# Optimization experiments

Measured on AMD Instinct MI355X. Metric: run time of the kernel, lower is better.

The kernel has to match this reference:

```python
import jax, jax.numpy as jnp
import numpy as np

C = 0.1          # curvature
EPS = 1e-8
BN_EPS = 1e-5
MAX_NORM = 0.9

def batchnorm_train(x, gamma, beta):
    mu = jnp.mean(x, axis=0)
    var = jnp.var(x, axis=0)  # biased, matches torch BN normalization
    return gamma * (x - mu) * jax.lax.rsqrt(var + BN_EPS) + beta

def euclidean_to_poincare(x, c=C, max_norm=MAX_NORM):
    norm = jnp.linalg.norm(x, axis=-1, keepdims=True)
    zeros_mask = norm == 0
    safe_norm = jnp.where(zeros_mask, jnp.ones_like(norm), norm)
    sqrt_c = jnp.sqrt(jnp.asarray(c, x.dtype))
    scale = max_norm * jnp.tanh(sqrt_c * norm) / (sqrt_c * safe_norm)
    return jnp.where(zeros_mask, jnp.zeros_like(x), scale * x)

def poincare_to_euclidean(x, c=C):
    norms = jnp.linalg.norm(x, axis=-1, keepdims=True)
    norms = jnp.clip(norms, 1e-8, 1.0 - 1e-8)
    sqrt_c = jnp.sqrt(jnp.asarray(c, x.dtype))
    return x * jnp.arctanh(sqrt_c * norms) / (sqrt_c * norms)

def batch_poincare_exp_map(x, v, c=C):
    x_nsq = jnp.sum(x * x, axis=-1, keepdims=True)
    lambda_x = 2.0 / (1.0 - c * x_nsq + EPS)
    v_norm = jnp.linalg.norm(v, axis=-1, keepdims=True)
    v_norm = jnp.maximum(v_norm, EPS)
    sqrt_c = jnp.sqrt(jnp.asarray(c, x.dtype))
    scale = jnp.tanh(sqrt_c * lambda_x * v_norm / 2.0) / (sqrt_c * v_norm)
    sv = scale * v
    numerator = (1.0 - c * x_nsq) * sv
    x_sv = jnp.sum(x * sv, axis=-1, keepdims=True)
    sv_nsq = jnp.sum(sv * sv, axis=-1, keepdims=True)
    denom = 1.0 - 2.0 * c * x_sv + c * c * x_nsq * sv_nsq
    result = x + numerator / (denom + EPS)
    mask = jnp.all(jnp.isfinite(result), axis=-1, keepdims=True)
    return jnp.where(mask, result, jnp.zeros_like(result))

def batch_poincare_log_map(x, y, c=C):
    x_nsq = jnp.sum(x * x, axis=-1, keepdims=True)
    lambda_x = 2.0 / (1.0 - c * x_nsq + EPS)
    y_nsq = jnp.sum(y * y, axis=-1, keepdims=True)
    xy = jnp.sum(x * y, axis=-1, keepdims=True)
    numerator = (1.0 - 2.0 * c * xy + c * y_nsq) * x - (1.0 - c * x_nsq) * y
    denom = 1.0 - 2.0 * c * xy + c * c * x_nsq * y_nsq
    diff = numerator / (denom + EPS)
    diff_norm = jnp.linalg.norm(diff, axis=-1, keepdims=True)
    diff_norm = jnp.maximum(diff_norm, EPS)
    sqrt_c = jnp.sqrt(jnp.asarray(c, x.dtype))
    return 2.0 / (sqrt_c * lambda_x) * jnp.arctanh(sqrt_c * diff_norm) * diff / diff_norm

def setup_inputs() -> dict:
    key = jax.random.key(0)
    ks = jax.random.split(key, 8)
    B, D_IN, H, D_OUT = 8192, 1024, 2048, 1000
    x = jax.random.normal(ks[0], (B, D_IN), dtype=jnp.float32)
    # kaiming_normal fan_out: std = sqrt(2/fan_out) with fan_out = out_features
    W1 = jax.random.normal(ks[1], (H, D_IN), dtype=jnp.float32) * np.sqrt(2.0 / H)
    b1 = jnp.zeros((H,), jnp.float32)
    g1 = jnp.ones((H,), jnp.float32)
    be1 = jnp.zeros((H,), jnp.float32)
    W2 = jax.random.normal(ks[2], (H, H), dtype=jnp.float32) * np.sqrt(2.0 / H)
    b2 = jnp.zeros((H,), jnp.float32)
    g2 = jnp.ones((H,), jnp.float32)
    be2 = jnp.zeros((H,), jnp.float32)
    W3 = jax.random.normal(ks[3], (D_OUT, H), dtype=jnp.float32) * np.sqrt(2.0 / D_OUT)
    b3 = jnp.zeros((D_OUT,), jnp.float32)
    return {"x": x, "W1": W1, "b1": b1, "g1": g1, "be1": be1,
            "W2": W2, "b2": b2, "g2": g2, "be2": be2, "W3": W3, "b3": b3}

def reference(x, W1, b1, g1, be1, W2, b2, g2, be2, W3, b3):
    h1 = jax.nn.relu(batchnorm_train(x @ W1.T + b1, g1, be1))
    h1_hyp = euclidean_to_poincare(h1)
    origin = jnp.zeros_like(h1_hyp)
    h1_tan = batch_poincare_log_map(origin, h1_hyp)
    h2_tan = jax.nn.relu(batchnorm_train(h1_tan @ W2.T + b2, g2, be2))
    h2_hyp = batch_poincare_exp_map(origin, h2_tan)
    h2_euc = poincare_to_euclidean(h2_hyp)
    out = h2_euc @ W3.T + b3
    return jax.nn.log_softmax(out, axis=1)
```

## Files before the change

### kernel.cpp

```cpp
#include <hip/hip_runtime.h>

typedef __bf16 bf16x8 __attribute__((ext_vector_type(8)));
typedef float f32x16 __attribute__((ext_vector_type(16)));
typedef unsigned short us8 __attribute__((ext_vector_type(8)));

#define AS1 __attribute__((address_space(1)))
#define AS3 __attribute__((address_space(3)))

__device__ __forceinline__ unsigned short f2bf(float x) {
  unsigned int u = __float_as_uint(x);
  u += 0x7fffu + ((u >> 16) & 1u);
  return (unsigned short)(u >> 16);
}
__device__ __forceinline__ float bf2f(unsigned short u) {
  return __uint_as_float(((unsigned int)u) << 16);
}
__device__ __forceinline__ void async_copy16(const void* g, void* l) {
  __builtin_amdgcn_global_load_lds((AS1 void*)(g), (AS3 void*)(l), 16, 0, 0);
}

#define BARRIER() asm volatile("s_barrier" ::: "memory")
#define WAITV(n) asm volatile("s_waitcnt vmcnt(" #n ")" ::: "memory")

__global__ void __launch_bounds__(256) k_prep(const float* __restrict__ x,
                                              const float* __restrict__ W1,
                                              const float* __restrict__ W2,
                                              const float* __restrict__ W3,
                                              unsigned short* __restrict__ Xb,
                                              unsigned short* __restrict__ W1b,
                                              unsigned short* __restrict__ W2b,
                                              unsigned short* __restrict__ W3b,
                                              float* __restrict__ P) {
  const long n1 = 2097152, n2 = 524288, n3 = 1048576, n4 = 524288;
  long i = (long)blockIdx.x * 256 + threadIdx.x;
  const float* s = nullptr;
  unsigned short* d = nullptr;
  long j = i;
  if (i < n1)                { s = x;  d = Xb; }
  else if ((j -= n1) < n2)   { s = W1; d = W1b; }
  else if ((j -= n2) < n3)   { s = W2; d = W2b; }
  else if ((j -= n3) < n4) {
    ushort4 o;
    if ((j >> 9) < 1000) {
      float4 v = ((const float4*)W3)[j];
      o.x = f2bf(v.x); o.y = f2bf(v.y); o.z = f2bf(v.z); o.w = f2bf(v.w);
    } else { o.x = 0; o.y = 0; o.z = 0; o.w = 0; }
    ((ushort4*)W3b)[j] = o;
    return;
  } else {
    j -= n4;
    ((float4*)P)[j] = (float4){0.f, 0.f, 0.f, 0.f};
    return;
  }
  float4 v = ((const float4*)s)[j];
  ushort4 o;
  o.x = f2bf(v.x); o.y = f2bf(v.y); o.z = f2bf(v.z); o.w = f2bf(v.w);
  ((ushort4*)d)[j] = o;
}

template <bool OUTBF16, bool STATS>
__global__ void __launch_bounds__(512, 2) k_gemm(const unsigned short* __restrict__ A,
                                                 const unsigned short* __restrict__ B,
                                                 void* __restrict__ Cout,
                                                 void* __restrict__ Cout2, int K,
                                                 int lda, int ldb, int ldc,
                                                 float* __restrict__ P) {
  __shared__ __align__(16) unsigned short lA[2][256 * 64];
  __shared__ __align__(16) unsigned short lB[2][256 * 64];
  const int tid = threadIdx.x;
  const int wave = tid >> 6;
  const int lane = tid & 63;
  const int l31 = lane & 31;
  const int khi = lane >> 5;
  const int r7 = l31 & 7;
  const int wrh = wave >> 2;
  const int wcn = wave & 3;

  const int f = blockIdx.x + gridDim.x * blockIdx.y;
  const int xcd = f & 7;
  const int fi = f >> 3;
  const int nblk = fi % gridDim.x;
  const int mblk = fi / gridDim.x + (gridDim.y >> 3) * xcd;
  const long m0 = (long)mblk * 256;
  const long n0 = (long)nblk * 256;
  const long koff = (long)blockIdx.z * K;
  const int NT = K >> 6;

  const int rsub = lane >> 3;
  const int qg = ((lane & 7) ^ rsub) * 8;
  const unsigned short* gAq0 = A + (m0 +       8 * wave + rsub) * (long)lda + koff + qg;
  const unsigned short* gAq1 = A + (m0 +  64 + 8 * wave + rsub) * (long)lda + koff + qg;
  const unsigned short* gAq2 = A + (m0 + 128 + 8 * wave + rsub) * (long)lda + koff + qg;
  const unsigned short* gAq3 = A + (m0 + 192 + 8 * wave + rsub) * (long)lda + koff + qg;
  const unsigned short* gB0  = B + (n0 + 32 * wave + rsub) * (long)ldb + koff + qg;
  const unsigned short* gB1  = gB0 +  8 * (long)ldb;
  const unsigned short* gB2  = gB0 + 16 * (long)ldb;
  const unsigned short* gB3  = gB0 + 24 * (long)ldb;
  const int dAq0 = (      8 * wave) * 64;
  const int dAq1 = ( 64 + 8 * wave) * 64;
  const int dAq2 = (128 + 8 * wave) * 64;
  const int dAq3 = (192 + 8 * wave) * 64;
  const int dB0  = (32 * wave) * 64;

  f32x16 acc[4][2];
#pragma unroll
  for (int i = 0; i < 4; ++i)
#pragma unroll
    for (int j = 0; j < 2; ++j) acc[i][j] = (f32x16)(0.f);

#define PH_READS(rh, kh, DOB)                                                        \
  bf16x8 af[2][2];                                                                   \
  _Pragma("unroll") for (int i = 0; i < 2; ++i) {                                    \
    _Pragma("unroll") for (int ks = 0; ks < 2; ++ks) {                               \
      af[i][ks] = *(const bf16x8*)&lAc[(wrh * 128 + (rh) * 64 + i * 32 + l31) * 64 + \
                                       ((((kh) * 2 + ks) * 2 + khi) ^ r7) * 8];      \
    }                                                                                \
  }                                                                                  \
  if (DOB) {                                                                         \
    _Pragma("unroll") for (int j = 0; j < 2; ++j) {                                  \
      _Pragma("unroll") for (int ks = 0; ks < 2; ++ks) {                             \
        bf[j][ks] = *(const bf16x8*)&lBc[(wcn * 64 + j * 32 + l31) * 64 +            \
                                         ((((kh) * 2 + ks) * 2 + khi) ^ r7) * 8];    \
      }                                                                              \
    }                                                                                \
  }

#define PH_MFMA(rh)                                                                 \
  __builtin_amdgcn_s_setprio(1);                                                    \
  _Pragma("unroll") for (int ks = 0; ks < 2; ++ks) {                                 \
    _Pragma("unroll") for (int i = 0; i < 2; ++i) {                                  \
      _Pragma("unroll") for (int j = 0; j < 2; ++j) {                                \
        acc[(rh) * 2 + i][j] = __builtin_amdgcn_mfma_f32_32x32x16_bf16(              \
            af[i][ks], bf[j][ks], acc[(rh) * 2 + i][j], 0, 0, 0);                    \
      }                                                                              \
    }                                                                                \
  }                                                                                  \
  __builtin_amdgcn_s_setprio(0);

  {
    unsigned short* lAn = &lA[0][0];
    unsigned short* lBn = &lB[0][0];
    async_copy16(gAq0, lAn + dAq0);
    async_copy16(gAq2, lAn + dAq2);
    async_copy16(gB0,  lBn + dB0);
    async_copy16(gB1,  lBn + dB0 + 8 * 64);
    async_copy16(gB2,  lBn + dB0 + 16 * 64);
    async_copy16(gB3,  lBn + dB0 + 24 * 64);
    async_copy16(gAq1, lAn + dAq1);
    async_copy16(gAq3, lAn + dAq3);
    WAITV(2);
    BARRIER();
  }

  for (int t = 0; t < NT - 1; ++t) {
    const unsigned short* lAc = &lA[t & 1][0];
    const unsigned short* lBc = &lB[t & 1][0];
    unsigned short* lAn = &lA[(t + 1) & 1][0];
    unsigned short* lBn = &lB[(t + 1) & 1][0];
    const long kk = (long)(t + 1) * 64;
    bf16x8 bf[2][2];
    {
      PH_READS(0, 0, 1)
      async_copy16(gAq0 + kk, lAn + dAq0);
      async_copy16(gAq2 + kk, lAn + dAq2);
      BARRIER();
      PH_MFMA(0)
      WAITV(2);
      BARRIER();
    }
    {
      PH_READS(1, 0, 0)
      async_copy16(gB0 + kk, lBn + dB0);
      async_copy16(gB1 + kk, lBn + dB0 + 8 * 64);
      BARRIER();
      PH_MFMA(1)
      BARRIER();
    }
    {
      PH_READS(0, 1, 1)
      async_copy16(gB2 + kk, lBn + dB0 + 16 * 64);
      async_copy16(gB3 + kk, lBn + dB0 + 24 * 64);
      BARRIER();
      PH_MFMA(0)
      BARRIER();
    }
    {
      PH_READS(1, 1, 0)
      async_copy16(gAq1 + kk, lAn + dAq1);
      async_copy16(gAq3 + kk, lAn + dAq3);
      BARRIER();
      PH_MFMA(1)
      WAITV(2);
      BARRIER();
    }
  }

  {
    const unsigned short* lAc = &lA[(NT - 1) & 1][0];
    const unsigned short* lBc = &lB[(NT - 1) & 1][0];
    bf16x8 bf[2][2];
    { PH_READS(0, 0, 1) BARRIER(); PH_MFMA(0) WAITV(0); BARRIER(); }
    { PH_READS(1, 0, 0) BARRIER(); PH_MFMA(1) BARRIER(); }
    { PH_READS(0, 1, 1) BARRIER(); PH_MFMA(0) BARRIER(); }
    { PH_READS(1, 1, 0) BARRIER(); PH_MFMA(1) BARRIER(); }
  }
#undef PH_READS
#undef PH_MFMA

  const int rbase = 4 * khi;
  const long crow0 = m0 + wrh * 128;
  const long ccol0 = n0 + wcn * 64;
  if (OUTBF16) {
    unsigned short* C = (unsigned short*)(blockIdx.z ? Cout2 : Cout);
#pragma unroll
    for (int ig = 0; ig < 4; ++ig)
#pragma unroll
      for (int j = 0; j < 2; ++j) {
        long col = ccol0 + j * 32 + l31;
#pragma unroll
        for (int reg = 0; reg < 16; ++reg) {
          long row = crow0 + ig * 32 + (reg & 3) + 8 * (reg >> 2) + rbase;
          C[row * (long)ldc + col] = f2bf(acc[ig][j][reg]);
        }
      }
  } else {
    float* C = (float*)(blockIdx.z ? Cout2 : Cout);
#pragma unroll
    for (int ig = 0; ig < 4; ++ig)
#pragma unroll
      for (int j = 0; j < 2; ++j) {
        long col = ccol0 + j * 32 + l31;
#pragma unroll
        for (int reg = 0; reg < 16; ++reg) {
          long row = crow0 + ig * 32 + (reg & 3) + 8 * (reg >> 2) + rbase;
          C[row * (long)ldc + col] = acc[ig][j][reg];
        }
      }
  }

  if (STATS) {
    float* sred = (float*)&lA[0][0];
    sred[tid] = 0.f;
    __syncthreads();
#pragma unroll
    for (int j = 0; j < 2; ++j) {
      float s = 0.f, s2 = 0.f;
#pragma unroll
      for (int ig = 0; ig < 4; ++ig)
#pragma unroll
        for (int reg = 0; reg < 16; ++reg) {
          float v = acc[ig][j][reg];
          s += v;
          s2 = fmaf(v, v, s2);
        }
      int cl = wcn * 64 + j * 32 + l31;
      atomicAdd(&sred[cl], s);
      atomicAdd(&sred[256 + cl], s2);
    }
    __syncthreads();
    if (tid < 256) atomicAdd(&P[n0 + tid], sred[tid]);
    else           atomicAdd(&P[2048 + n0 + tid - 256], sred[tid]);
  }
}

template <bool STAGE2>
__global__ void __launch_bounds__(256) k_fuse(const unsigned short* __restrict__ Zb,
                                              const float* __restrict__ P,
                                              const float* __restrict__ g,
                                              const float* __restrict__ be,
                                              unsigned short* __restrict__ Ab) {
  const int t = threadIdx.x, wave = t >> 6, lane = t & 63;
  const long row = (long)blockIdx.x * 4 + wave;

  float sc[32], sh[32];
#pragma unroll
  for (int c = 0; c < 4; ++c) {
    int b4 = (lane + 64 * c) * 2;
    float4 s0 = ((const float4*)P)[b4],       s1 = ((const float4*)P)[b4 + 1];
    float4 q0 = ((const float4*)P)[512 + b4], q1 = ((const float4*)P)[512 + b4 + 1];
    float4 g0 = ((const float4*)g)[b4],       g1 = ((const float4*)g)[b4 + 1];
    float4 e0 = ((const float4*)be)[b4],      e1 = ((const float4*)be)[b4 + 1];
    float sm[8] = {s0.x, s0.y, s0.z, s0.w, s1.x, s1.y, s1.z, s1.w};
    float sq[8] = {q0.x, q0.y, q0.z, q0.w, q1.x, q1.y, q1.z, q1.w};
    float gg[8] = {g0.x, g0.y, g0.z, g0.w, g1.x, g1.y, g1.z, g1.w};
    float bb[8] = {e0.x, e0.y, e0.z, e0.w, e1.x, e1.y, e1.z, e1.w};
#pragma unroll
    for (int j = 0; j < 8; ++j) {
      float mean = sm[j] * (1.f / 8192.f);
      float var = sq[j] * (1.f / 8192.f) - mean * mean;
      float a = gg[j] * rsqrtf(var + 1e-5f);
      sc[c * 8 + j] = a;
      sh[c * 8 + j] = bb[j] - mean * a;
    }
  }

  const us8* zr = (const us8*)(Zb + row * 2048);
  float v[32];
  float ss = 0.f;
#pragma unroll
  for (int c = 0; c < 4; ++c) {
    us8 z8 = zr[lane + 64 * c];
#pragma unroll
    for (int j = 0; j < 8; ++j) {
      float xv = fmaxf(fmaf(bf2f(z8[j]), sc[c * 8 + j], sh[c * 8 + j]), 0.f);
      v[c * 8 + j] = xv;
      ss = fmaf(xv, xv, ss);
    }
  }
#pragma unroll
  for (int o = 32; o > 0; o >>= 1) ss += __shfl_xor(ss, o, 64);
  float n2 = ss;

  const float rsc = 0.31622776601683794f;
  float fac;
  if (STAGE2) {
    float nn = sqrtf(n2);
    float vn = fmaxf(nn, 1e-8f);
    float tt = rsc * vn;
    float scl = tanhf(tt) / tt;
    float hn = scl * nn;
    float cn = fminf(fmaxf(hn, 1e-8f), 1.0f);
    float z = rsc * cn;
    fac = scl * (atanhf(z) / z);
  } else {
    fac = 0.f;
    if (n2 > 0.f) {
      float n = sqrtf(n2);
      float th = tanhf(rsc * n);
      float s = 0.9f * th / (rsc * n);
      float dn = fmaxf(s * n, 1e-8f);
      float z = rsc * dn;
      fac = -(atanhf(z) / z) * s;
    }
  }
  us8* dr = (us8*)(Ab + row * 2048);
#pragma unroll
  for (int c = 0; c < 4; ++c) {
    us8 o8;
#pragma unroll
    for (int j = 0; j < 8; ++j) o8[j] = f2bf(v[c * 8 + j] * fac);
    dr[lane + 64 * c] = o8;
  }
}

__global__ void __launch_bounds__(256) k_lsm(const unsigned short* __restrict__ Za,
                                             const unsigned short* __restrict__ Zb2,
                                             const float* __restrict__ b3,
                                             float* __restrict__ out) {
  const int t = threadIdx.x, wave = t >> 6, lane = t & 63;
  const long row = (long)blockIdx.x * 4 + wave;
  const unsigned short* za = Za + row * 1024;
  const unsigned short* zb = Zb2 + row * 1024;
  float v[16];
  float mx = -3.4e38f;
#pragma unroll
  for (int c = 0; c < 16; ++c) {
    int col = lane + 64 * c;
    if (col < 1000) {
      v[c] = bf2f(za[col]) + bf2f(zb[col]) + b3[col];
      mx = fmaxf(mx, v[c]);
    } else v[c] = -3.4e38f;
  }
#pragma unroll
  for (int o = 32; o > 0; o >>= 1) mx = fmaxf(mx, __shfl_xor(mx, o, 64));

  float se = 0.f;
#pragma unroll
  for (int c = 0; c < 16; ++c) {
    int col = lane + 64 * c;
    if (col < 1000) se += expf(v[c] - mx);
  }
#pragma unroll
  for (int o = 32; o > 0; o >>= 1) se += __shfl_xor(se, o, 64);
  float ls = logf(se);

  float* orow = out + row * 1000;
#pragma unroll
  for (int c = 0; c < 16; ++c) {
    int col = lane + 64 * c;
    if (col < 1000) orow[col] = v[c] - mx - ls;
  }
}

extern "C" void kernel_launch(void* const* d_in, const int* in_sizes, int n_in,
                              void* d_out, int out_size, void* d_ws, size_t ws_size,
                              hipStream_t stream) {
  (void)in_sizes; (void)n_in; (void)out_size; (void)ws_size;
  const float* x   = (const float*)d_in[0];
  const float* W1  = (const float*)d_in[1];
  const float* g1  = (const float*)d_in[3];
  const float* be1 = (const float*)d_in[4];
  const float* W2  = (const float*)d_in[5];
  const float* g2  = (const float*)d_in[7];
  const float* be2 = (const float*)d_in[8];
  const float* W3  = (const float*)d_in[9];
  const float* b3  = (const float*)d_in[10];
  float* out = (float*)d_out;

  char* ws = (char*)d_ws;
  size_t off = 0;
  auto alloc = [&](size_t bytes) {
    void* p = ws + off;
    off += (bytes + 255) & ~(size_t)255;
    return p;
  };
  unsigned short* Xb  = (unsigned short*)alloc((size_t)8192 * 1024 * 2);
  unsigned short* W1b = (unsigned short*)alloc((size_t)2048 * 1024 * 2);
  unsigned short* W2b = (unsigned short*)alloc((size_t)2048 * 2048 * 2);
  unsigned short* W3b = (unsigned short*)alloc((size_t)1024 * 2048 * 2);
  unsigned short* Zb  = (unsigned short*)alloc((size_t)8192 * 2048 * 2);
  unsigned short* Ab  = (unsigned short*)alloc((size_t)8192 * 2048 * 2);
  unsigned short* Z3a = (unsigned short*)alloc((size_t)8192 * 1024 * 2);
  float* P            = (float*)alloc((size_t)2 * 4096 * 4);
  float* P2 = P + 4096;
  unsigned short* Z3b = Zb;

  k_prep<<<16392, 256, 0, stream>>>(x, W1, W2, W3, Xb, W1b, W2b, W3b, P);

  k_gemm<true, true><<<dim3(8, 32, 1), 512, 0, stream>>>(Xb, W1b, Zb, Zb, 1024, 1024, 1024, 2048, P);
  k_fuse<false><<<2048, 256, 0, stream>>>(Zb, P, g1, be1, Ab);

  k_gemm<true, true><<<dim3(8, 32, 1), 512, 0, stream>>>(Ab, W2b, Zb, Zb, 2048, 2048, 2048, 2048, P2);
  k_fuse<true><<<2048, 256, 0, stream>>>(Zb, P2, g2, be2, Ab);

  k_gemm<true, false><<<dim3(4, 32, 2), 512, 0, stream>>>(Ab, W3b, Z3a, Z3b, 1024, 2048, 2048, 1024, nullptr);
  k_lsm<<<2048, 256, 0, stream>>>(Z3a, Z3b, b3, out);
}
```

Baseline: 317.6 us.

## Switch GEMM from 32x32x16 to 16x16x32 MFMA with new LDS swizzle

Replaces the 32x32x16 bf16 MFMA tiling with 16x16x32 MFMAs, reorganizing per-wave fragments into 8x4 accumulators of 4 floats. The LDS swizzle pattern and global-to-LDS column permutation are changed to match the new lane-to-k mapping. The epilogue and BN statistics reduction are remapped to the new accumulator layout. The new XOR swizzle only flips one bit, so LDS bank conflicts may rise and trade against any gain in MFMA issue efficiency.

```diff
diff --git a/kernel.cpp b/kernel.cpp
--- a/kernel.cpp
+++ b/kernel.cpp
@@ -1,7 +1,7 @@
 #include <hip/hip_runtime.h>
 
 typedef __bf16 bf16x8 __attribute__((ext_vector_type(8)));
-typedef float f32x16 __attribute__((ext_vector_type(16)));
+typedef float f32x4 __attribute__((ext_vector_type(4)));
 typedef unsigned short us8 __attribute__((ext_vector_type(8)));
 
 #define AS1 __attribute__((address_space(1)))
@@ -70,9 +70,9 @@
   const int tid = threadIdx.x;
   const int wave = tid >> 6;
   const int lane = tid & 63;
-  const int l31 = lane & 31;
-  const int khi = lane >> 5;
-  const int r7 = l31 & 7;
+  const int l15 = lane & 15;
+  const int kc = lane >> 4;
+  const int sw2 = ((lane >> 2) & 1) << 1;
   const int wrh = wave >> 2;
   const int wcn = wave & 3;
 
@@ -87,7 +87,7 @@
   const int NT = K >> 6;
 
   const int rsub = lane >> 3;
-  const int qg = ((lane & 7) ^ rsub) * 8;
+  const int qg = ((lane & 7) ^ (((lane >> 5) & 1) << 1)) * 8;
   const unsigned short* gAq0 = A + (m0 +       8 * wave + rsub) * (long)lda + koff + qg;
   const unsigned short* gAq1 = A + (m0 +  64 + 8 * wave + rsub) * (long)lda + koff + qg;
   const unsigned short* gAq2 = A + (m0 + 128 + 8 * wave + rsub) * (long)lda + koff + qg;
@@ -102,37 +102,31 @@
   const int dAq3 = (192 + 8 * wave) * 64;
   const int dB0  = (32 * wave) * 64;
 
-  f32x16 acc[4][2];
-#pragma unroll
-  for (int i = 0; i < 4; ++i)
-#pragma unroll
-    for (int j = 0; j < 2; ++j) acc[i][j] = (f32x16)(0.f);
+  f32x4 acc[8][4];
+#pragma unroll
+  for (int i = 0; i < 8; ++i)
+#pragma unroll
+    for (int j = 0; j < 4; ++j) acc[i][j] = (f32x4)(0.f);
 
 #define PH_READS(rh, kh, DOB)                                                        \
-  bf16x8 af[2][2];                                                                   \
-  _Pragma("unroll") for (int i = 0; i < 2; ++i) {                                    \
-    _Pragma("unroll") for (int ks = 0; ks < 2; ++ks) {                               \
-      af[i][ks] = *(const bf16x8*)&lAc[(wrh * 128 + (rh) * 64 + i * 32 + l31) * 64 + \
-                                       ((((kh) * 2 + ks) * 2 + khi) ^ r7) * 8];      \
-    }                                                                                \
+  bf16x8 af[4];                                                                      \
+  _Pragma("unroll") for (int m = 0; m < 4; ++m) {                                    \
+    af[m] = *(const bf16x8*)&lAc[(wrh * 128 + (rh) * 64 + m * 16 + l15) * 64 +       \
+                                 ((((kh) * 4 + kc) ^ sw2) * 8)];                     \
   }                                                                                  \
   if (DOB) {                                                                         \
-    _Pragma("unroll") for (int j = 0; j < 2; ++j) {                                  \
-      _Pragma("unroll") for (int ks = 0; ks < 2; ++ks) {                             \
-        bf[j][ks] = *(const bf16x8*)&lBc[(wcn * 64 + j * 32 + l31) * 64 +            \
-                                         ((((kh) * 2 + ks) * 2 + khi) ^ r7) * 8];    \
-      }                                                                              \
+    _Pragma("unroll") for (int n = 0; n < 4; ++n) {                                  \
+      bf[n] = *(const bf16x8*)&lBc[(wcn * 64 + n * 16 + l15) * 64 +                  \
+                                   ((((kh) * 4 + kc) ^ sw2) * 8)];                   \
     }                                                                                \
   }
 
 #define PH_MFMA(rh)                                                                 \
   __builtin_amdgcn_s_setprio(1);                                                    \
-  _Pragma("unroll") for (int ks = 0; ks < 2; ++ks) {                                 \
-    _Pragma("unroll") for (int i = 0; i < 2; ++i) {                                  \
-      _Pragma("unroll") for (int j = 0; j < 2; ++j) {                                \
-        acc[(rh) * 2 + i][j] = __builtin_amdgcn_mfma_f32_32x32x16_bf16(              \
-            af[i][ks], bf[j][ks], acc[(rh) * 2 + i][j], 0, 0, 0);                    \
-      }                                                                              \
+  _Pragma("unroll") for (int m = 0; m < 4; ++m) {                                    \
+    _Pragma("unroll") for (int n = 0; n < 4; ++n) {                                  \
+      acc[(rh) * 4 + m][n] = __builtin_amdgcn_mfma_f32_16x16x32_bf16(                \
+          af[m], bf[n], acc[(rh) * 4 + m][n], 0, 0, 0);                              \
     }                                                                                \
   }                                                                                  \
   __builtin_amdgcn_s_setprio(0);
@@ -158,7 +152,7 @@
     unsigned short* lAn = &lA[(t + 1) & 1][0];
     unsigned short* lBn = &lB[(t + 1) & 1][0];
     const long kk = (long)(t + 1) * 64;
-    bf16x8 bf[2][2];
+    bf16x8 bf[4];
     {
       PH_READS(0, 0, 1)
       async_copy16(gAq0 + kk, lAn + dAq0);
@@ -198,7 +192,7 @@
   {
     const unsigned short* lAc = &lA[(NT - 1) & 1][0];
     const unsigned short* lBc = &lB[(NT - 1) & 1][0];
-    bf16x8 bf[2][2];
+    bf16x8 bf[4];
     { PH_READS(0, 0, 1) BARRIER(); PH_MFMA(0) WAITV(0); BARRIER(); }
     { PH_READS(1, 0, 0) BARRIER(); PH_MFMA(1) BARRIER(); }
     { PH_READS(0, 1, 1) BARRIER(); PH_MFMA(0) BARRIER(); }
@@ -207,33 +201,32 @@
 #undef PH_READS
 #undef PH_MFMA
 
-  const int rbase = 4 * khi;
   const long crow0 = m0 + wrh * 128;
   const long ccol0 = n0 + wcn * 64;
   if (OUTBF16) {
     unsigned short* C = (unsigned short*)(blockIdx.z ? Cout2 : Cout);
 #pragma unroll
-    for (int ig = 0; ig < 4; ++ig)
-#pragma unroll
-      for (int j = 0; j < 2; ++j) {
-        long col = ccol0 + j * 32 + l31;
-#pragma unroll
-        for (int reg = 0; reg < 16; ++reg) {
-          long row = crow0 + ig * 32 + (reg & 3) + 8 * (reg >> 2) + rbase;
-          C[row * (long)ldc + col] = f2bf(acc[ig][j][reg]);
+    for (int m = 0; m < 8; ++m)
+#pragma unroll
+      for (int n = 0; n < 4; ++n) {
+        long col = ccol0 + n * 16 + l15;
+#pragma unroll
+        for (int reg = 0; reg < 4; ++reg) {
+          long row = crow0 + m * 16 + kc * 4 + reg;
+          C[row * (long)ldc + col] = f2bf(acc[m][n][reg]);
         }
       }
   } else {
     float* C = (float*)(blockIdx.z ? Cout2 : Cout);
 #pragma unroll
-    for (int ig = 0; ig < 4; ++ig)
-#pragma unroll
-      for (int j = 0; j < 2; ++j) {
-        long col = ccol0 + j * 32 + l31;
-#pragma unroll
-        for (int reg = 0; reg < 16; ++reg) {
-          long row = crow0 + ig * 32 + (reg & 3) + 8 * (reg >> 2) + rbase;
-          C[row * (long)ldc + col] = acc[ig][j][reg];
+    for (int m = 0; m < 8; ++m)
+#pragma unroll
+      for (int n = 0; n < 4; ++n) {
+        long col = ccol0 + n * 16 + l15;
+#pragma unroll
+        for (int reg = 0; reg < 4; ++reg) {
+          long row = crow0 + m * 16 + kc * 4 + reg;
+          C[row * (long)ldc + col] = acc[m][n][reg];
         }
       }
   }
@@ -243,17 +236,17 @@
     sred[tid] = 0.f;
     __syncthreads();
 #pragma unroll
-    for (int j = 0; j < 2; ++j) {
+    for (int n = 0; n < 4; ++n) {
       float s = 0.f, s2 = 0.f;
 #pragma unroll
-      for (int ig = 0; ig < 4; ++ig)
-#pragma unroll
-        for (int reg = 0; reg < 16; ++reg) {
-          float v = acc[ig][j][reg];
+      for (int m = 0; m < 8; ++m)
+#pragma unroll
+        for (int reg = 0; reg < 4; ++reg) {
+          float v = acc[m][n][reg];
           s += v;
           s2 = fmaf(v, v, s2);
         }
-      int cl = wcn * 64 + j * 32 + l31;
+      int cl = wcn * 64 + n * 16 + l15;
       atomicAdd(&sred[cl], s);
       atomicAdd(&sred[256 + cl], s2);
     }
```

Measured after the change: 313.3 us. No clear change (-1.3%).
